# Performance work log

Hardware: AMD Instinct MI355X
Metric: run time of the kernel (lower is better)

The kernel has to match this reference:

```python
import jax, jax.numpy as jnp
import numpy as np

N, R, L, H, D, E = 30000, 3, 4, 128, 128, 20000  # nodes, ranks, max group len, hidden, input_dim, n_hyperedges
NUM_HEADS = 4


def _xavier(rng, fan_in, fan_out, shape=None):
    bound = np.sqrt(6.0 / (fan_in + fan_out))
    shape = (fan_in, fan_out) if shape is None else shape
    return jnp.asarray(rng.uniform(-bound, bound, size=shape), dtype=jnp.float32)


def setup_inputs() -> dict:
    rng = np.random.default_rng(0)
    # hyperedge id h has rank h % R; ids of rank r are r + R*k
    deg = 1 + (np.arange(N * R).reshape(N, R) % L)          # per (node, rank) group size in 1..L
    mask = np.arange(L)[None, None, :] < deg[:, :, None]    # [N,R,L] valid slots
    ks = rng.integers(0, E // R, size=(N, R, L))
    he_idx = ks * R + np.arange(R)[None, :, None]           # hyperedge ids matching each rank row
    he_idx = np.where(mask, he_idx, 0)
    valid_idx = np.flatnonzero(mask.reshape(-1)).astype(np.int64)  # [nnz], nnz = 225000
    # he_order: per-node argsort of its (rank-ordered) valid hyperedge id list, plus running offset
    flatm = mask.reshape(N, R * L)
    row_vals = np.where(flatm, he_idx.reshape(N, R * L), E + 1)
    perm = np.argsort(row_vals, axis=1, kind='stable')      # positions of sorted values
    compact = np.cumsum(flatm, axis=1) - 1                   # padded pos -> compact (valid-list) index
    deg_total = flatm.sum(1)
    offsets = np.concatenate([[0], np.cumsum(deg_total)[:-1]])
    compact_at_perm = np.take_along_axis(compact, perm, axis=1)
    take = np.arange(R * L)[None, :] < deg_total[:, None]
    he_order = (compact_at_perm + offsets[:, None])[take].astype(np.int64)
    inp = {
        'x_rank': jnp.asarray(rng.standard_normal((N, R, D)), jnp.float32),
        'he_features': jnp.asarray(rng.standard_normal((E, H)), jnp.float32),
        'he_idx': jnp.asarray(he_idx, jnp.int32),
        'valid_idx': jnp.asarray(valid_idx, jnp.int32),
        'he_order': jnp.asarray(he_order, jnp.int32),
        # GRU gate parameters (whh: hidden->hidden, wxh: input->hidden, b: hidden)
        'r_whh': _xavier(rng, H, H), 'r_wxh': _xavier(rng, D, H), 'r_b': jnp.zeros((H,), jnp.float32),
        'u_whh': _xavier(rng, H, H), 'u_wxh': _xavier(rng, D, H), 'u_b': jnp.zeros((H,), jnp.float32),
        'c_whh': _xavier(rng, H, H), 'c_wxh': _xavier(rng, D, H), 'c_b': jnp.zeros((H,), jnp.float32),
        # MultiheadAttention params (torch layout: in_proj_weight [3H,H])
        'in_proj_w': _xavier(rng, 3 * H, H, shape=(3 * H, H)),
        'in_proj_b': jnp.zeros((3 * H,), jnp.float32),
        'out_w': _xavier(rng, H, H, shape=(H, H)),
        'out_b': jnp.zeros((H,), jnp.float32),
    }
    return inp


def reference(x_rank, he_features, he_idx, valid_idx, he_order,
              r_whh, r_wxh, r_b, u_whh, u_wxh, u_b, c_whh, c_wxh, c_b,
              in_proj_w, in_proj_b, out_w, out_b):
    n, n_ranks, _ = x_rank.shape
    hd = H // NUM_HEADS

    # ---- GRU over ranks (sequence axis) ----
    def step(h, x_t):
        r = jax.nn.sigmoid(h @ r_whh + x_t @ r_wxh + r_b)
        z = jax.nn.sigmoid(h @ u_whh + x_t @ u_wxh + u_b)
        c = jnp.tanh((r * h) @ c_whh + x_t @ c_wxh + c_b)  # (r*h)@W per python precedence
        h = z * c + (1.0 - z) * h
        return h, h

    h0 = jnp.zeros((n, H), x_rank.dtype)
    _, hs = jax.lax.scan(step, h0, jnp.swapaxes(x_rank, 0, 1))  # [R,N,H]
    hs = jnp.swapaxes(hs, 0, 1)                                  # [N,R,H]

    # ---- ragged gather-pad + per (node, rank) MHA with a single key/value ----
    wq, wk, wv = in_proj_w[:H], in_proj_w[H:2 * H], in_proj_w[2 * H:]
    bq, bk, bv = in_proj_b[:H], in_proj_b[H:2 * H], in_proj_b[2 * H:]
    q = he_features[he_idx]                                       # [N,R,L,H]
    qp = (q @ wq.T + bq).reshape(n, n_ranks, L, NUM_HEADS, hd)
    kp = (hs @ wk.T + bk).reshape(n, n_ranks, NUM_HEADS, hd)
    vp = (hs @ wv.T + bv).reshape(n, n_ranks, NUM_HEADS, hd)
    scale = 1.0 / jnp.sqrt(jnp.asarray(hd, q.dtype))
    scores = jnp.einsum('nrlhd,nrhd->nrlh', qp, kp) * scale       # key length is 1
    attn = jax.nn.softmax(scores[..., None], axis=-1)[..., 0]     # softmax over singleton key axis -> 1
    ctx = attn[..., None] * vp[:, :, None]                        # [N,R,L,heads,hd]
    out = ctx.reshape(n, n_ranks, L, H) @ out_w.T + out_b         # [N,R,L,H]
    # select valid (non-padded) slots, concatenated in node/rank order
    result = out.reshape(-1, H)[valid_idx]                        # [nnz,H]
    return result, he_order
```

## Files before the change

### kernel.cpp

```cpp
#include <hip/hip_runtime.h>
#include <math.h>

#define Hd 128
#define Rr 3
#define Ll 4
#define NPW 16
#define NW  8

typedef float f32x4 __attribute__((ext_vector_type(4)));
typedef short s16x8 __attribute__((ext_vector_type(8)));

__device__ __forceinline__ unsigned short f2bf(float f){
    unsigned u = __float_as_uint(f);
    return (unsigned short)((u + 0x7FFFu + ((u >> 16) & 1u)) >> 16);
}
__device__ __forceinline__ float bf2f(unsigned short h){
    return __uint_as_float(((unsigned)h) << 16);
}
__device__ __forceinline__ s16x8 cvt8(const float* p){
    float4 a = *(const float4*)p;
    float4 b = *(const float4*)(p + 4);
    float v[8] = {a.x, a.y, a.z, a.w, b.x, b.y, b.z, b.w};
    s16x8 r;
    #pragma unroll
    for (int j = 0; j < 8; ++j) r[j] = (short)f2bf(v[j]);
    return r;
}
__device__ __forceinline__ int lower_bound_i32(const int* __restrict__ a, int n, int key){
    int lo = 0, hi = n;
    while (lo < hi){
        int mid = (lo + hi) >> 1;
        if (a[mid] < key) lo = mid + 1; else hi = mid;
    }
    return lo;
}
__device__ __forceinline__ void gload_lds16(const unsigned short* g, unsigned short* l){
    __builtin_amdgcn_global_load_lds(
        (const __attribute__((address_space(1))) void*)g,
        (__attribute__((address_space(3))) void*)l, 16, 0, 0);
}
__device__ __forceinline__ float gxel(uint2 u, int i){
    unsigned w = (i < 2) ? u.x : u.y;
    return bf2f((unsigned short)((i & 1) ? (w >> 16) : (w & 0xffff)));
}

__global__ void fold_proj_kernel(const float* __restrict__ in_proj_w,
                                 const float* __restrict__ in_proj_b,
                                 const float* __restrict__ out_w,
                                 const float* __restrict__ out_b,
                                 float* __restrict__ McT,
                                 float* __restrict__ bc)
{
    const int i = blockIdx.x;
    const int j = threadIdx.x;
    float acc = 0.f;
    for (int k = 0; k < Hd; ++k)
        acc = fmaf(out_w[j * Hd + k], in_proj_w[(2 * Hd + k) * Hd + i], acc);
    McT[i * Hd + j] = acc;
    if (i == 0){
        float b = out_b[j];
        for (int k = 0; k < Hd; ++k)
            b = fmaf(out_w[j * Hd + k], in_proj_b[2 * Hd + k], b);
        bc[j] = b;
    }
}

__global__ void pack_kernel(const float* __restrict__ r_whh, const float* __restrict__ u_whh,
                            const float* __restrict__ r_wxh, const float* __restrict__ u_wxh,
                            const float* __restrict__ c_whh, const float* __restrict__ c_wxh,
                            const float* __restrict__ McT,
                            unsigned short* __restrict__ whi)
{
    const int mat  = blockIdx.y;
    const int tile = blockIdx.x;
    const int l    = threadIdx.x;
    const float* W;
    switch (mat){
        case 0: W = r_whh; break;  case 1: W = u_whh; break;
        case 2: W = r_wxh; break;  case 3: W = u_wxh; break;
        case 4: W = c_whh; break;  case 5: W = c_wxh; break;
        default: W = McT;
    }
    const int kc = tile >> 3, nc = tile & 7;
    const int kbase = kc * 32 + (l >> 4) * 8;
    const int n = nc * 16 + (l & 15);
    const size_t obase = ((size_t)(mat * 32 + tile) * 64 + l) * 8;
    #pragma unroll
    for (int j = 0; j < 8; ++j)
        whi[obase + j] = f2bf(W[(kbase + j) * Hd + n]);
}

#define MM1(acc, AH, BH)                                                  \
    acc = __builtin_amdgcn_mfma_f32_16x16x32_bf16(AH, BH, acc, 0, 0, 0);

__global__ __launch_bounds__(512, 1) void gx_kernel(
    const float* __restrict__ x_rank,
    const float* __restrict__ r_b, const float* __restrict__ u_b, const float* __restrict__ c_b,
    const unsigned short* __restrict__ whi,
    uint2* __restrict__ gx, int N, int NT)
{
    __shared__ __align__(16) unsigned short WX[3][16384];
    const int tid = threadIdx.x;
    const int wid = tid >> 6;
    const int l   = tid & 63;
    const int lr  = l & 15;
    const int lg  = l >> 4;

    const int mats[3] = {2, 3, 5};
    #pragma unroll
    for (int m = 0; m < 3; ++m){
        const unsigned short* msrc = whi + (size_t)mats[m] * 16384;
        #pragma unroll
        for (int it = 0; it < 4; ++it){
            const int chunk = it * 8 + wid;
            gload_lds16(msrc + chunk * 512 + l * 8, &WX[m][chunk * 512]);
        }
    }
    __syncthreads();

    const int u = blockIdx.x * NW + wid;
    if (u >= 3 * NT) return;
    const int t  = u / NT;
    const int nt = u % NT;

    int nn = nt * NPW + lr; if (nn > N - 1) nn = N - 1;
    const float* xp = x_rank + ((size_t)nn * Rr + t) * Hd;
    s16x8 xh[4];
    #pragma unroll
    for (int kc = 0; kc < 4; ++kc)
        xh[kc] = cvt8(xp + kc * 32 + lg * 8);

    #pragma unroll
    for (int g = 0; g < 3; ++g){
        const float* bp = (g == 0) ? r_b : (g == 1) ? u_b : c_b;
        #pragma unroll
        for (int nc = 0; nc < 8; ++nc){
            f32x4 acc = (f32x4){0.f, 0.f, 0.f, 0.f};
            #pragma unroll
            for (int kc = 0; kc < 4; ++kc){
                s16x8 b = *(const s16x8*)&WX[g][(((kc) * 8 + nc) * 64 + l) * 8];
                MM1(acc, xh[kc], b);
            }
            const float bb = bp[nc * 16 + lr];
            uint2 o;
            o.x = ((unsigned)f2bf(acc[1] + bb) << 16) | f2bf(acc[0] + bb);
            o.y = ((unsigned)f2bf(acc[3] + bb) << 16) | f2bf(acc[2] + bb);
            gx[(((size_t)(g * Rr + t) * NT + nt) * 8 + nc) * 64 + l] = o;
            if ((nc & 3) == 3) __builtin_amdgcn_sched_barrier(0);
        }
    }
}

#define BF_LDS(kc, nc) (*(const s16x8*)&WL[cur][(((kc) * 8 + (nc)) * 64 + l) * 8])
#define GXLD(g, t, nc) gx[(((size_t)((g) * Rr + (t)) * NT + gtile) * 8 + (nc)) * 64 + l]

__global__ __launch_bounds__(512, 1) void gru_rec9_kernel(
    const int* __restrict__ valid_idx, int nv,
    const unsigned short* __restrict__ whi,
    const uint2* __restrict__ gx,
    const float* __restrict__ bc,
    float* __restrict__ out, int N, int NT)
{
    __shared__ __align__(16) unsigned short WL[2][16384];
    __shared__ __align__(16) float Sr_all[NW][NPW][132];
    __shared__ int lo_all[NW][NPW];
    __shared__ int hi_all[NW][NPW];

    const int tid = threadIdx.x;
    const int wid = tid >> 6;
    const int l   = tid & 63;
    const int lr  = l & 15;
    const int lg  = l >> 4;
    const int wtile = blockIdx.x * NW + wid;
    const int n0  = wtile * NPW;
    const int gtile = (wtile < NT) ? wtile : NT - 1;

    float (*Sr)[132] = Sr_all[wid];
    int* loL = lo_all[wid];
    int* hiL = hi_all[wid];

    #define STAGE_MAT(mat, b)                                                    \
        {                                                                        \
            const unsigned short* msrc = whi + (size_t)(mat) * 16384;            \
            _Pragma("unroll")                                                    \
            for (int it = 0; it < 4; ++it){                                      \
                const int chunk = it * 8 + wid;                                  \
                gload_lds16(msrc + chunk * 512 + l * 8, &WL[b][chunk * 512]);    \
            }                                                                    \
        }

    f32x4 hD[8];
    s16x8 ah[4], rhh[4];
    f32x4 zD[8];
    float obc[8];
    #pragma unroll
    for (int nc = 0; nc < 8; ++nc) obc[nc] = bc[nc * 16 + lr];

    unsigned cur = 0;
    STAGE_MAT(6, 0);

    #pragma unroll 1
    for (int t = 0; t < Rr; ++t){
        if (l < NPW){
            int n = n0 + l, lo = 0, hi = 0;
            if (n < N){
                int F = (n * Rr + t) * Ll;
                lo = lower_bound_i32(valid_idx, nv, F);
                hi = lower_bound_i32(valid_idx, nv, F + Ll);
            }
            loL[l] = lo; hiL[l] = hi;
        }

        if (t == 0){
            uint2 gu[8], gc[8];
            #pragma unroll
            for (int nc = 0; nc < 8; ++nc){ gu[nc] = GXLD(1, 0, nc); gc[nc] = GXLD(2, 0, nc); }
            #pragma unroll
            for (int nc = 0; nc < 8; ++nc){
                #pragma unroll
                for (int i = 0; i < 4; ++i){
                    float z = 1.f / (1.f + __expf(-gxel(gu[nc], i)));
                    float e = __expf(2.f * gxel(gc[nc], i));
                    float c = 1.f - 2.f / (e + 1.f);
                    float hn = z * c;
                    hD[nc][i] = hn;
                    Sr[lg * 4 + i][nc * 16 + lr] = hn;
                }
            }
            #pragma unroll
            for (int kc = 0; kc < 4; ++kc)
                ah[kc] = cvt8(&Sr[lr][kc * 32 + lg * 8]);
        } else {
            __syncthreads();
            STAGE_MAT(1, cur ^ 1);
            uint2 gr[8];
            #pragma unroll
            for (int nc = 0; nc < 8; ++nc) gr[nc] = GXLD(0, t, nc);
            #pragma unroll
            for (int nc = 0; nc < 8; ++nc){
                f32x4 accR = (f32x4){0.f, 0.f, 0.f, 0.f};
                #pragma unroll
                for (int kc = 0; kc < 4; ++kc){ s16x8 b = BF_LDS(kc, nc); MM1(accR, ah[kc], b); }
                #pragma unroll
                for (int i = 0; i < 4; ++i){
                    float r = 1.f / (1.f + __expf(-(accR[i] + gxel(gr[nc], i))));
                    Sr[lg * 4 + i][nc * 16 + lr] = r * hD[nc][i];
                }
                if ((nc & 3) == 3) __builtin_amdgcn_sched_barrier(0);
            }
            cur ^= 1;

            __syncthreads();
            STAGE_MAT(4, cur ^ 1);
            uint2 gu[8];
            #pragma unroll
            for (int nc = 0; nc < 8; ++nc) gu[nc] = GXLD(1, t, nc);
            #pragma unroll
            for (int nc = 0; nc < 8; ++nc){
                f32x4 accZ = (f32x4){0.f, 0.f, 0.f, 0.f};
                #pragma unroll
                for (int kc = 0; kc < 4; ++kc){ s16x8 b = BF_LDS(kc, nc); MM1(accZ, ah[kc], b); }
                #pragma unroll
                for (int i = 0; i < 4; ++i)
                    zD[nc][i] = 1.f / (1.f + __expf(-(accZ[i] + gxel(gu[nc], i))));
                if ((nc & 3) == 3) __builtin_amdgcn_sched_barrier(0);
            }
            #pragma unroll
            for (int kc = 0; kc < 4; ++kc)
                rhh[kc] = cvt8(&Sr[lr][kc * 32 + lg * 8]);
            cur ^= 1;

            __syncthreads();
            STAGE_MAT(6, cur ^ 1);
            uint2 gc[8];
            #pragma unroll
            for (int nc = 0; nc < 8; ++nc) gc[nc] = GXLD(2, t, nc);
            #pragma unroll
            for (int nc = 0; nc < 8; ++nc){
                f32x4 accC = (f32x4){0.f, 0.f, 0.f, 0.f};
                #pragma unroll
                for (int kc = 0; kc < 4; ++kc){ s16x8 b = BF_LDS(kc, nc); MM1(accC, rhh[kc], b); }
                #pragma unroll
                for (int i = 0; i < 4; ++i){
                    float e = __expf(2.f * (accC[i] + gxel(gc[nc], i)));
                    float c = 1.f - 2.f / (e + 1.f);
                    float ho = hD[nc][i];
                    float hn = ho + zD[nc][i] * (c - ho);
                    hD[nc][i] = hn;
                    Sr[lg * 4 + i][nc * 16 + lr] = hn;
                }
                if ((nc & 3) == 3) __builtin_amdgcn_sched_barrier(0);
            }
            #pragma unroll
            for (int kc = 0; kc < 4; ++kc)
                ah[kc] = cvt8(&Sr[lr][kc * 32 + lg * 8]);
            cur ^= 1;
        }

        __syncthreads();
        if (t < Rr - 1) STAGE_MAT(0, cur ^ 1);
        #pragma unroll
        for (int nc = 0; nc < 8; ++nc){
            f32x4 ao = (f32x4){0.f, 0.f, 0.f, 0.f};
            #pragma unroll
            for (int kc = 0; kc < 4; ++kc){ s16x8 b = BF_LDS(kc, nc); MM1(ao, ah[kc], b); }
            #pragma unroll
            for (int i = 0; i < 4; ++i)
                Sr[lg * 4 + i][nc * 16 + lr] = ao[i] + obc[nc];
            if ((nc & 3) == 3) __builtin_amdgcn_sched_barrier(0);
        }
        #pragma unroll
        for (int m = 0; m < 8; ++m){
            const int row = m * 2 + (l >> 5);
            const int c4  = (l & 31) * 4;
            const float4 v = *(const float4*)&Sr[row][c4];
            const int lo = loL[row], hi = hiL[row];
            for (int rr = lo; rr < hi; ++rr)
                *(float4*)(out + (size_t)rr * Hd + c4) = v;
        }
        cur ^= 1;
    }
    #undef STAGE_MAT
}

__global__ __launch_bounds__(512, 1) void gru_mfma_fb(
    const float* __restrict__ x_rank,
    const int* __restrict__ valid_idx, int nv,
    const float* __restrict__ r_b, const float* __restrict__ u_b, const float* __restrict__ c_b,
    const unsigned short* __restrict__ whi,
    const float* __restrict__ bc,
    float* __restrict__ out, int N)
{
    __shared__ __align__(16) unsigned short WL[2][16384];
    __shared__ __align__(16) float Sr_all[NW][NPW][132];
    __shared__ float bias_s[4][Hd];
    __shared__ int lo_all[NW][NPW];
    __shared__ int hi_all[NW][NPW];

    const int tid = threadIdx.x;
    const int wid = tid >> 6;
    const int l   = tid & 63;
    const int lr  = l & 15;
    const int lg  = l >> 4;
    const int n0  = (blockIdx.x * NW + wid) * NPW;

    float (*Sr)[132] = Sr_all[wid];
    int* loL = lo_all[wid];
    int* hiL = hi_all[wid];

    if (tid < Hd){
        bias_s[0][tid] = r_b[tid];
        bias_s[1][tid] = u_b[tid];
        bias_s[2][tid] = c_b[tid];
        bias_s[3][tid] = bc[tid];
    }
    #define STAGE_MAT(mat, b)                                                    \
        {                                                                        \
            const unsigned short* msrc = whi + (size_t)(mat) * 16384;            \
            _Pragma("unroll")                                                    \
            for (int it = 0; it < 4; ++it){                                      \
                const int chunk = it * 8 + wid;                                  \
                gload_lds16(msrc + chunk * 512 + l * 8, &WL[b][chunk * 512]);    \
            }                                                                    \
        }
    f32x4 hD[8];
    s16x8 ah[4];
    #pragma unroll
    for (int nc = 0; nc < 8; ++nc) hD[nc] = (f32x4){0.f, 0.f, 0.f, 0.f};
    #pragma unroll
    for (int kc = 0; kc < 4; ++kc) ah[kc] = (s16x8)0;
    s16x8 xh[4], rhh[4];

    unsigned cur = 0;
    STAGE_MAT(0, 0);

    #pragma unroll 1
    for (int t = 0; t < Rr; ++t){
        if (l < NPW){
            int n = n0 + l, lo = 0, hi = 0;
            if (n < N){
                int F = (n * Rr + t) * Ll;
                lo = lower_bound_i32(valid_idx, nv, F);
                hi = lower_bound_i32(valid_idx, nv, F + Ll);
            }
            loL[l] = lo; hiL[l] = hi;
        }
        {
            int nn = n0 + lr; if (nn > N - 1) nn = N - 1;
            const float* xp = x_rank + ((size_t)nn * Rr + t) * Hd;
            #pragma unroll
            for (int kc = 0; kc < 4; ++kc)
                xh[kc] = cvt8(xp + kc * 32 + lg * 8);
        }
        f32x4 accR[8], accZ[8];
        __syncthreads();
        STAGE_MAT(2, cur ^ 1);
        #pragma unroll
        for (int nc = 0; nc < 8; ++nc){
            accR[nc] = (f32x4){0.f, 0.f, 0.f, 0.f};
            #pragma unroll
            for (int kc = 0; kc < 4; ++kc){ s16x8 b = BF_LDS(kc, nc); MM1(accR[nc], ah[kc], b); }
            if ((nc & 3) == 3) __builtin_amdgcn_sched_barrier(0);
        }
        cur ^= 1;
        __syncthreads();
        STAGE_MAT(1, cur ^ 1);
        #pragma unroll
        for (int nc = 0; nc < 8; ++nc){
            #pragma unroll
            for (int kc = 0; kc < 4; ++kc){ s16x8 b = BF_LDS(kc, nc); MM1(accR[nc], xh[kc], b); }
            const float rbc = bias_s[0][nc * 16 + lr];
            #pragma unroll
            for (int i = 0; i < 4; ++i){
                float r = 1.f / (1.f + __expf(-(accR[nc][i] + rbc)));
                Sr[lg * 4 + i][nc * 16 + lr] = r * hD[nc][i];
            }
            if ((nc & 3) == 3) __builtin_amdgcn_sched_barrier(0);
        }
        cur ^= 1;
        __syncthreads();
        STAGE_MAT(3, cur ^ 1);
        #pragma unroll
        for (int nc = 0; nc < 8; ++nc){
            accZ[nc] = (f32x4){0.f, 0.f, 0.f, 0.f};
            #pragma unroll
            for (int kc = 0; kc < 4; ++kc){ s16x8 b = BF_LDS(kc, nc); MM1(accZ[nc], ah[kc], b); }
            if ((nc & 3) == 3) __builtin_amdgcn_sched_barrier(0);
        }
        cur ^= 1;
        __syncthreads();
        STAGE_MAT(4, cur ^ 1);
        #pragma unroll
        for (int nc = 0; nc < 8; ++nc){
            #pragma unroll
            for (int kc = 0; kc < 4; ++kc){ s16x8 b = BF_LDS(kc, nc); MM1(accZ[nc], xh[kc], b); }
            const float ubc = bias_s[1][nc * 16 + lr];
            #pragma unroll
            for (int i = 0; i < 4; ++i)
                accZ[nc][i] = 1.f / (1.f + __expf(-(accZ[nc][i] + ubc)));
            if ((nc & 3) == 3) __builtin_amdgcn_sched_barrier(0);
        }
        cur ^= 1;
        __syncthreads();
        STAGE_MAT(5, cur ^ 1);
        #pragma unroll
        for (int kc = 0; kc < 4; ++kc)
            rhh[kc] = cvt8(&Sr[lr][kc * 32 + lg * 8]);
        f32x4 accC[8];
        #pragma unroll
        for (int nc = 0; nc < 8; ++nc){
            accC[nc] = (f32x4){0.f, 0.f, 0.f, 0.f};
            #pragma unroll
            for (int kc = 0; kc < 4; ++kc){ s16x8 b = BF_LDS(kc, nc); MM1(accC[nc], rhh[kc], b); }
            if ((nc & 3) == 3) __builtin_amdgcn_sched_barrier(0);
        }
        cur ^= 1;
        __syncthreads();
        STAGE_MAT(6, cur ^ 1);
        #pragma unroll
        for (int nc = 0; nc < 8; ++nc){
            #pragma unroll
            for (int kc = 0; kc < 4; ++kc){ s16x8 b = BF_LDS(kc, nc); MM1(accC[nc], xh[kc], b); }
            const float cbc = bias_s[2][nc * 16 + lr];
            #pragma unroll
            for (int i = 0; i < 4; ++i){
                float e = __expf(2.f * (accC[nc][i] + cbc));
                float c = 1.f - 2.f / (e + 1.f);
                float ho = hD[nc][i];
                float hn = ho + accZ[nc][i] * (c - ho);
                hD[nc][i] = hn;
                Sr[lg * 4 + i][nc * 16 + lr] = hn;
            }
            if ((nc & 3) == 3) __builtin_amdgcn_sched_barrier(0);
        }
        #pragma unroll
        for (int kc = 0; kc < 4; ++kc)
            ah[kc] = cvt8(&Sr[lr][kc * 32 + lg * 8]);
        cur ^= 1;
        __syncthreads();
        if (t < Rr - 1) STAGE_MAT(0, cur ^ 1);
        #pragma unroll
        for (int nc = 0; nc < 8; ++nc){
            f32x4 ao = (f32x4){0.f, 0.f, 0.f, 0.f};
            #pragma unroll
            for (int kc = 0; kc < 4; ++kc){ s16x8 b = BF_LDS(kc, nc); MM1(ao, ah[kc], b); }
            const float obc = bias_s[3][nc * 16 + lr];
            #pragma unroll
            for (int i = 0; i < 4; ++i)
                Sr[lg * 4 + i][nc * 16 + lr] = ao[i] + obc;
            if ((nc & 3) == 3) __builtin_amdgcn_sched_barrier(0);
        }
        #pragma unroll
        for (int m = 0; m < 8; ++m){
            const int row = m * 2 + (l >> 5);
            const int c4  = (l & 31) * 4;
            const float4 v = *(const float4*)&Sr[row][c4];
            const int lo = loL[row], hi = hiL[row];
            for (int rr = lo; rr < hi; ++rr)
                *(float4*)(out + (size_t)rr * Hd + c4) = v;
        }
        cur ^= 1;
    }
    #undef STAGE_MAT
}

__global__ void he_order_kernel(const int* __restrict__ he_order,
                                float* __restrict__ out_tail, int nv)
{
    const int i = blockIdx.x * 256 + threadIdx.x;
    if (i < nv) out_tail[i] = (float)he_order[i];
}

extern "C" void kernel_launch(void* const* d_in, const int* in_sizes, int n_in,
                              void* d_out, int out_size, void* d_ws, size_t ws_size,
                              hipStream_t stream)
{
    const float* x_rank    = (const float*)d_in[0];
    const int*   valid_idx = (const int*)d_in[3];
    const int*   he_order  = (const int*)d_in[4];
    const float* r_whh = (const float*)d_in[5];
    const float* r_wxh = (const float*)d_in[6];
    const float* r_b   = (const float*)d_in[7];
    const float* u_whh = (const float*)d_in[8];
    const float* u_wxh = (const float*)d_in[9];
    const float* u_b   = (const float*)d_in[10];
    const float* c_whh = (const float*)d_in[11];
    const float* c_wxh = (const float*)d_in[12];
    const float* c_b   = (const float*)d_in[13];
    const float* in_proj_w = (const float*)d_in[14];
    const float* in_proj_b = (const float*)d_in[15];
    const float* out_w     = (const float*)d_in[16];
    const float* out_b     = (const float*)d_in[17];

    const int nv = in_sizes[3];
    const int N  = in_sizes[0] / (Rr * Hd);
    const int NT = (N + NPW - 1) / NPW;

    float* McT = (float*)d_ws;
    float* bc  = McT + Hd * Hd;
    unsigned short* whi = (unsigned short*)(bc + Hd);
    const size_t base = 16384*4 + 128*4 + 7*16384*2;
    uint2* gx = (uint2*)((char*)d_ws + base);
    const size_t gx_bytes = (size_t)9 * NT * 8 * 64 * 8;

    float* out_f    = (float*)d_out;
    float* out_tail = out_f + (size_t)nv * Hd;

    fold_proj_kernel<<<Hd, Hd, 0, stream>>>(in_proj_w, in_proj_b, out_w, out_b, McT, bc);
    pack_kernel<<<dim3(32, 7), 64, 0, stream>>>(r_whh, u_whh, r_wxh, u_wxh, c_whh, c_wxh,
                                                McT, whi);

    const int nodes_per_block = NW * NPW;
    const int nblocks = (N + nodes_per_block - 1) / nodes_per_block;

    if (ws_size >= base + gx_bytes){
        const int gxblocks = (3 * NT + NW - 1) / NW;
        gx_kernel<<<gxblocks, 512, 0, stream>>>(x_rank, r_b, u_b, c_b, whi, gx, N, NT);
        gru_rec9_kernel<<<nblocks, 512, 0, stream>>>(valid_idx, nv, whi, gx, bc, out_f, N, NT);
    } else {
        gru_mfma_fb<<<nblocks, 512, 0, stream>>>(
            x_rank, valid_idx, nv, r_b, u_b, c_b, whi, bc, out_f, N);
    }

    he_order_kernel<<<(nv + 255) / 256, 256, 0, stream>>>(he_order, out_tail, nv);
}
```

Measured before the change: 105.4 us.

## Fuse projection fold into pack, merge he_order copy into gx kernel, prefetch gates

The separate fold_proj kernel is removed and the folded out_w·Wv product is computed directly inside pack_kernel (mat 6), with a new mat 7 slice computing the bias. The he_order conversion is appended as extra blocks of the gx kernel, which drops a launch. The gx kernel now double-buffers its three weight matrices in LDS (two buffers instead of three) and skips storing the unused t=0 r-gate. The recurrence kernel also issues all three gate gx loads up front. The aim is fewer launches, lower LDS use and hidden gx load latency, at the cost of redundant per-element dot products in pack and higher register pressure in the recurrence.

Result: slower. 120.5 us (+14.4%).

```diff
diff --git a/kernel.cpp b/kernel.cpp
--- a/kernel.cpp
+++ b/kernel.cpp
@@ -44,47 +44,54 @@
     return bf2f((unsigned short)((i & 1) ? (w >> 16) : (w & 0xffff)));
 }
 
-__global__ void fold_proj_kernel(const float* __restrict__ in_proj_w,
-                                 const float* __restrict__ in_proj_b,
-                                 const float* __restrict__ out_w,
-                                 const float* __restrict__ out_b,
-                                 float* __restrict__ McT,
-                                 float* __restrict__ bc)
-{
-    const int i = blockIdx.x;
-    const int j = threadIdx.x;
-    float acc = 0.f;
-    for (int k = 0; k < Hd; ++k)
-        acc = fmaf(out_w[j * Hd + k], in_proj_w[(2 * Hd + k) * Hd + i], acc);
-    McT[i * Hd + j] = acc;
-    if (i == 0){
-        float b = out_b[j];
-        for (int k = 0; k < Hd; ++k)
-            b = fmaf(out_w[j * Hd + k], in_proj_b[2 * Hd + k], b);
-        bc[j] = b;
-    }
-}
-
 __global__ void pack_kernel(const float* __restrict__ r_whh, const float* __restrict__ u_whh,
                             const float* __restrict__ r_wxh, const float* __restrict__ u_wxh,
                             const float* __restrict__ c_whh, const float* __restrict__ c_wxh,
-                            const float* __restrict__ McT,
-                            unsigned short* __restrict__ whi)
+                            const float* __restrict__ in_proj_w, const float* __restrict__ in_proj_b,
+                            const float* __restrict__ out_w, const float* __restrict__ out_b,
+                            unsigned short* __restrict__ whi, float* __restrict__ bc)
 {
     const int mat  = blockIdx.y;
     const int tile = blockIdx.x;
     const int l    = threadIdx.x;
+
+    if (mat == 7){
+        if (tile == 0){
+            #pragma unroll
+            for (int h = 0; h < 2; ++h){
+                const int j = l + h * 64;
+                float b = out_b[j];
+                for (int k = 0; k < Hd; ++k)
+                    b = fmaf(out_w[j * Hd + k], in_proj_b[2 * Hd + k], b);
+                bc[j] = b;
+            }
+        }
+        return;
+    }
+
+    const int kc = tile >> 3, nc = tile & 7;
+    const int kbase = kc * 32 + (l >> 4) * 8;
+    const int n = nc * 16 + (l & 15);
+    const size_t obase = ((size_t)(mat * 32 + tile) * 64 + l) * 8;
+
+    if (mat == 6){
+        #pragma unroll
+        for (int j = 0; j < 8; ++j){
+            const int ki = kbase + j;
+            float acc = 0.f;
+            for (int k = 0; k < Hd; ++k)
+                acc = fmaf(out_w[n * Hd + k], in_proj_w[(2 * Hd + k) * Hd + ki], acc);
+            whi[obase + j] = f2bf(acc);
+        }
+        return;
+    }
+
     const float* W;
     switch (mat){
         case 0: W = r_whh; break;  case 1: W = u_whh; break;
         case 2: W = r_wxh; break;  case 3: W = u_wxh; break;
-        case 4: W = c_whh; break;  case 5: W = c_wxh; break;
-        default: W = McT;
-    }
-    const int kc = tile >> 3, nc = tile & 7;
-    const int kbase = kc * 32 + (l >> 4) * 8;
-    const int n = nc * 16 + (l & 15);
-    const size_t obase = ((size_t)(mat * 32 + tile) * 64 + l) * 8;
+        case 4: W = c_whh; break;  default: W = c_wxh;
+    }
     #pragma unroll
     for (int j = 0; j < 8; ++j)
         whi[obase + j] = f2bf(W[(kbase + j) * Hd + n]);
@@ -93,35 +100,45 @@
 #define MM1(acc, AH, BH)                                                  \
     acc = __builtin_amdgcn_mfma_f32_16x16x32_bf16(AH, BH, acc, 0, 0, 0);
 
-__global__ __launch_bounds__(512, 1) void gx_kernel(
+__global__ __launch_bounds__(512, 1) void gx_he_kernel(
     const float* __restrict__ x_rank,
     const float* __restrict__ r_b, const float* __restrict__ u_b, const float* __restrict__ c_b,
     const unsigned short* __restrict__ whi,
-    uint2* __restrict__ gx, int N, int NT)
+    uint2* __restrict__ gx, int N, int NT, int gxblocks,
+    const int* __restrict__ he_order, float* __restrict__ out_tail, int nv)
 {
-    __shared__ __align__(16) unsigned short WX[3][16384];
     const int tid = threadIdx.x;
+
+    const int hb = (int)blockIdx.x - gxblocks;
+    if (hb >= 0){
+        const int i = hb * 512 + tid;
+        if (i < nv) out_tail[i] = (float)he_order[i];
+        return;
+    }
+
+    __shared__ __align__(16) unsigned short WX[2][16384];
     const int wid = tid >> 6;
     const int l   = tid & 63;
     const int lr  = l & 15;
     const int lg  = l >> 4;
 
-    const int mats[3] = {2, 3, 5};
-    #pragma unroll
-    for (int m = 0; m < 3; ++m){
-        const unsigned short* msrc = whi + (size_t)mats[m] * 16384;
-        #pragma unroll
-        for (int it = 0; it < 4; ++it){
-            const int chunk = it * 8 + wid;
-            gload_lds16(msrc + chunk * 512 + l * 8, &WX[m][chunk * 512]);
-        }
-    }
-    __syncthreads();
+    #define STAGE_X(mat, b)                                                      \
+        {                                                                        \
+            const unsigned short* msrc = whi + (size_t)(mat) * 16384;            \
+            _Pragma("unroll")                                                    \
+            for (int it = 0; it < 4; ++it){                                      \
+                const int chunk = it * 8 + wid;                                  \
+                gload_lds16(msrc + chunk * 512 + l * 8, &WX[b][chunk * 512]);    \
+            }                                                                    \
+        }
+
+    STAGE_X(2, 0);
 
     const int u = blockIdx.x * NW + wid;
-    if (u >= 3 * NT) return;
-    const int t  = u / NT;
-    const int nt = u % NT;
+    const int valid = (u < 3 * NT);
+    const int uu = valid ? u : 3 * NT - 1;
+    const int t  = uu / NT;
+    const int nt = uu % NT;
 
     int nn = nt * NPW + lr; if (nn > N - 1) nn = N - 1;
     const float* xp = x_rank + ((size_t)nn * Rr + t) * Hd;
@@ -130,25 +147,36 @@
     for (int kc = 0; kc < 4; ++kc)
         xh[kc] = cvt8(xp + kc * 32 + lg * 8);
 
-    #pragma unroll
-    for (int g = 0; g < 3; ++g){
-        const float* bp = (g == 0) ? r_b : (g == 1) ? u_b : c_b;
-        #pragma unroll
-        for (int nc = 0; nc < 8; ++nc){
-            f32x4 acc = (f32x4){0.f, 0.f, 0.f, 0.f};
-            #pragma unroll
-            for (int kc = 0; kc < 4; ++kc){
-                s16x8 b = *(const s16x8*)&WX[g][(((kc) * 8 + nc) * 64 + l) * 8];
-                MM1(acc, xh[kc], b);
-            }
-            const float bb = bp[nc * 16 + lr];
-            uint2 o;
-            o.x = ((unsigned)f2bf(acc[1] + bb) << 16) | f2bf(acc[0] + bb);
-            o.y = ((unsigned)f2bf(acc[3] + bb) << 16) | f2bf(acc[2] + bb);
-            gx[(((size_t)(g * Rr + t) * NT + nt) * 8 + nc) * 64 + l] = o;
-            if ((nc & 3) == 3) __builtin_amdgcn_sched_barrier(0);
-        }
-    }
+    #define GX_COMP(g, b, bp)                                                    \
+        {                                                                        \
+            _Pragma("unroll")                                                    \
+            for (int nc = 0; nc < 8; ++nc){                                      \
+                f32x4 acc = (f32x4){0.f, 0.f, 0.f, 0.f};                         \
+                _Pragma("unroll")                                                \
+                for (int kc = 0; kc < 4; ++kc){                                  \
+                    s16x8 bb = *(const s16x8*)&WX[b][(((kc) * 8 + nc) * 64 + l) * 8]; \
+                    MM1(acc, xh[kc], bb);                                        \
+                }                                                                \
+                const float bv = bp[nc * 16 + lr];                               \
+                uint2 o;                                                         \
+                o.x = ((unsigned)f2bf(acc[1] + bv) << 16) | f2bf(acc[0] + bv);   \
+                o.y = ((unsigned)f2bf(acc[3] + bv) << 16) | f2bf(acc[2] + bv);   \
+                if (valid && ((g) != 0 || t != 0))                               \
+                    gx[(((size_t)((g) * Rr + t) * NT + nt) * 8 + nc) * 64 + l] = o; \
+                if ((nc & 3) == 3) __builtin_amdgcn_sched_barrier(0);            \
+            }                                                                    \
+        }
+
+    __syncthreads();
+    STAGE_X(3, 1);
+    GX_COMP(0, 0, r_b);
+    __syncthreads();
+    STAGE_X(5, 0);
+    GX_COMP(1, 1, u_b);
+    __syncthreads();
+    GX_COMP(2, 0, c_b);
+    #undef GX_COMP
+    #undef STAGE_X
 }
 
 #define BF_LDS(kc, nc) (*(const s16x8*)&WL[cur][(((kc) * 8 + (nc)) * 64 + l) * 8])
@@ -231,11 +259,16 @@
             for (int kc = 0; kc < 4; ++kc)
                 ah[kc] = cvt8(&Sr[lr][kc * 32 + lg * 8]);
         } else {
+            uint2 gr[8], gu[8], gc[8];
+            #pragma unroll
+            for (int nc = 0; nc < 8; ++nc){
+                gr[nc] = GXLD(0, t, nc);
+                gu[nc] = GXLD(1, t, nc);
+                gc[nc] = GXLD(2, t, nc);
+            }
+
             __syncthreads();
             STAGE_MAT(1, cur ^ 1);
-            uint2 gr[8];
-            #pragma unroll
-            for (int nc = 0; nc < 8; ++nc) gr[nc] = GXLD(0, t, nc);
             #pragma unroll
             for (int nc = 0; nc < 8; ++nc){
                 f32x4 accR = (f32x4){0.f, 0.f, 0.f, 0.f};
@@ -252,9 +285,6 @@
 
             __syncthreads();
             STAGE_MAT(4, cur ^ 1);
-            uint2 gu[8];
-            #pragma unroll
-            for (int nc = 0; nc < 8; ++nc) gu[nc] = GXLD(1, t, nc);
             #pragma unroll
             for (int nc = 0; nc < 8; ++nc){
                 f32x4 accZ = (f32x4){0.f, 0.f, 0.f, 0.f};
@@ -272,9 +302,6 @@
 
             __syncthreads();
             STAGE_MAT(6, cur ^ 1);
-            uint2 gc[8];
-            #pragma unroll
-            for (int nc = 0; nc < 8; ++nc) gc[nc] = GXLD(2, t, nc);
             #pragma unroll
             for (int nc = 0; nc < 8; ++nc){
                 f32x4 accC = (f32x4){0.f, 0.f, 0.f, 0.f};
@@ -536,31 +563,31 @@
     const int N  = in_sizes[0] / (Rr * Hd);
     const int NT = (N + NPW - 1) / NPW;
 
-    float* McT = (float*)d_ws;
-    float* bc  = McT + Hd * Hd;
-    unsigned short* whi = (unsigned short*)(bc + Hd);
-    const size_t base = 16384*4 + 128*4 + 7*16384*2;
+    float* bc = (float*)d_ws;
+    unsigned short* whi = (unsigned short*)(bc + 128);
+    const size_t base = ((size_t)128 * 4 + 7 * 16384 * 2 + 255) & ~(size_t)255;
     uint2* gx = (uint2*)((char*)d_ws + base);
     const size_t gx_bytes = (size_t)9 * NT * 8 * 64 * 8;
 
     float* out_f    = (float*)d_out;
     float* out_tail = out_f + (size_t)nv * Hd;
 
-    fold_proj_kernel<<<Hd, Hd, 0, stream>>>(in_proj_w, in_proj_b, out_w, out_b, McT, bc);
-    pack_kernel<<<dim3(32, 7), 64, 0, stream>>>(r_whh, u_whh, r_wxh, u_wxh, c_whh, c_wxh,
-                                                McT, whi);
+    pack_kernel<<<dim3(32, 8), 64, 0, stream>>>(
+        r_whh, u_whh, r_wxh, u_wxh, c_whh, c_wxh,
+        in_proj_w, in_proj_b, out_w, out_b, whi, bc);
 
     const int nodes_per_block = NW * NPW;
     const int nblocks = (N + nodes_per_block - 1) / nodes_per_block;
 
     if (ws_size >= base + gx_bytes){
-        const int gxblocks = (3 * NT + NW - 1) / NW;
-        gx_kernel<<<gxblocks, 512, 0, stream>>>(x_rank, r_b, u_b, c_b, whi, gx, N, NT);
+        const int gxb = (3 * NT + NW - 1) / NW;
+        const int heb = (nv + 511) / 512;
+        gx_he_kernel<<<gxb + heb, 512, 0, stream>>>(
+            x_rank, r_b, u_b, c_b, whi, gx, N, NT, gxb, he_order, out_tail, nv);
         gru_rec9_kernel<<<nblocks, 512, 0, stream>>>(valid_idx, nv, whi, gx, bc, out_f, N, NT);
     } else {
         gru_mfma_fb<<<nblocks, 512, 0, stream>>>(
             x_rank, valid_idx, nv, r_b, u_b, c_b, whi, bc, out_f, N);
-    }
-
-    he_order_kernel<<<(nv + 255) / 256, 256, 0, stream>>>(he_order, out_tail, nv);
-}
+        he_order_kernel<<<(nv + 255) / 256, 256, 0, stream>>>(he_order, out_tail, nv);
+    }
+}
```
